# Optimization experiments

Measured on AMD Instinct MI355X. Metric: run time of the kernel, lower is better.

Reference implementation:

```python
import jax, jax.numpy as jnp
import numpy as np

MAXDISP = 25               # module stores maxdisp + 1
OFFSET = (MAXDISP - 1) // 2  # center of the residual disparity range


def setup_inputs() -> dict:
    key = jax.random.key(0)
    k1, k2 = jax.random.split(key)
    x = jax.random.normal(k1, (8, 32, 256, 512), dtype=jnp.float32)
    y = jax.random.normal(k2, (8, 32, 256, 512), dtype=jnp.float32)
    return {"x": x, "y": y}


def reference(x, y):
    # Residual cost volume: for each centered disparity shift d, the cost slice
    # is the channel-wise L1 distance between x and y shifted by d along width,
    # with zeros in the out-of-overlap columns.
    N, C, H, W = x.shape
    slices = []
    for i in range(MAXDISP):  # small fixed loop over disparity hypotheses
        d = i - OFFSET
        if d < 0:
            # overlap occupies columns [0, W+d); right -d columns are zero
            c = jnp.abs(x[..., : W + d] - y[..., -d:]).sum(axis=1)
            c = jnp.pad(c, ((0, 0), (0, 0), (0, -d)))
        elif d > 0:
            # overlap occupies columns [d, W); left d columns are zero
            c = jnp.abs(x[..., d:] - y[..., : W - d]).sum(axis=1)
            c = jnp.pad(c, ((0, 0), (0, 0), (d, 0)))
        else:
            c = jnp.abs(x - y).sum(axis=1)
        slices.append(c)  # (N, H, W)
    return jnp.stack(slices, axis=1)  # (N, MAXDISP, H, W)
```

## Files before the change

kernel.cpp:

```cpp
#include <hip/hip_runtime.h>

namespace {
constexpr int N_ = 8, C_ = 32, H_ = 256, W_ = 512, DISP_ = 25;
constexpr int CH = H_ * W_;
constexpr int TILE = 256;
constexpr int NSS = C_ / 2;
constexpr int YST = 288;
constexpr int YOFF = 256;
constexpr int BUF = 560;
}

typedef __attribute__((ext_vector_type(2))) _Float16 h2;

__device__ __forceinline__ h2 u2h(unsigned u) { return __builtin_bit_cast(h2, u); }
__device__ __forceinline__ unsigned h2u(h2 v) { return __builtin_bit_cast(unsigned, v); }

template <int G>
__device__ __forceinline__ void body(const float* px, const float* py0,
                                     const float* py1, bool extra,
                                     float* __restrict__ op, unsigned* lds,
                                     int tid, int w0l, int w0g) {
  constexpr int I0 = (G == 0) ? 0 : (G == 1) ? 7 : (G == 2) ? 13 : 19;
  constexpr int NI = (G == 0) ? 7 : 6;
  constexpr int OFF = (G == 0) ? 4 : (G == 1) ? 0 : (G == 2) ? -8 : -12;

  const h2 one = {(_Float16)1.0f, (_Float16)1.0f};

  float acc[NI][4];
#pragma unroll
  for (int il = 0; il < NI; ++il)
#pragma unroll
    for (int cw = 0; cw < 4; ++cw) acc[il][cw] = 0.0f;

  float a0, a1, b0, b1, c0, c1;

#define SLOAD()                                                           \
  do {                                                                    \
    a0 = px[0]; a1 = px[CH];                                              \
    b0 = py0[0]; b1 = py0[CH];                                            \
    if (extra) { c0 = py1[0]; c1 = py1[CH]; }                             \
    px += 2 * CH; py0 += 2 * CH; py1 += 2 * CH;                           \
  } while (0)

#define SWRITE(bsel)                                                      \
  do {                                                                    \
    unsigned* wp = lds + (bsel)*BUF;                                      \
    h2 pa = __builtin_bit_cast(h2, __builtin_amdgcn_cvt_pkrtz(a0, a1));   \
    h2 pb = __builtin_bit_cast(h2, __builtin_amdgcn_cvt_pkrtz(b0, b1));   \
    wp[tid] = h2u(pa);                                                    \
    wp[YOFF + tid] = h2u(pb);                                             \
    if (extra) {                                                          \
      h2 pc = __builtin_bit_cast(h2, __builtin_amdgcn_cvt_pkrtz(c0, c1)); \
      wp[YOFF + 256 + tid] = h2u(pc);                                     \
    }                                                                     \
  } while (0)

#define COMPUTE(bsel)                                                     \
  do {                                                                    \
    const unsigned* bp = lds + (bsel)*BUF;                                \
    const uint4 xq = *reinterpret_cast<const uint4*>(bp + w0l);           \
    const uint4 q0 = *reinterpret_cast<const uint4*>(bp + YOFF + w0l +    \
                                                     (OFF + 12));         \
    const uint4 q1 = *reinterpret_cast<const uint4*>(bp + YOFF + w0l +    \
                                                     (OFF + 12) + 4);    \
    const uint4 q2 = *reinterpret_cast<const uint4*>(bp + YOFF + w0l +    \
                                                     (OFF + 12) + 8);    \
    const unsigned xs[4] = {xq.x, xq.y, xq.z, xq.w};                      \
    const unsigned yw[12] = {q0.x, q0.y, q0.z, q0.w, q1.x, q1.y, q1.z,    \
                             q1.w, q2.x, q2.y, q2.z, q2.w};               \
    _Pragma("unroll") for (int il = 0; il < NI; ++il) {                   \
      _Pragma("unroll") for (int cw = 0; cw < 4; ++cw) {                  \
        h2 d = u2h(xs[cw]) - u2h(yw[cw + 12 - (I0 + il) - OFF]);          \
        h2 a = u2h(h2u(d) & 0x7FFF7FFFu);                                 \
        acc[il][cw] = __builtin_amdgcn_fdot2(a, one, acc[il][cw], false); \
      }                                                                   \
    }                                                                     \
  } while (0)

  SLOAD();
  SWRITE(0);
  __syncthreads();

  int cb = 0;
#pragma unroll 1
  for (int s = 0; s < NSS; ++s) {
    const bool more = (s + 1 < NSS);
    if (more) SLOAD();
    COMPUTE(cb);
    if (more) SWRITE(cb ^ 1);
    __syncthreads();
    cb ^= 1;
  }

#undef SLOAD
#undef SWRITE
#undef COMPUTE

#pragma unroll
  for (int il = 0; il < NI; ++il) {
    const int i = I0 + il;
    const int j0 = w0g - i + 12;
    float4 v;
    v.x = ((unsigned)(j0 + 0) < (unsigned)W_) ? acc[il][0] : 0.0f;
    v.y = ((unsigned)(j0 + 1) < (unsigned)W_) ? acc[il][1] : 0.0f;
    v.z = ((unsigned)(j0 + 2) < (unsigned)W_) ? acc[il][2] : 0.0f;
    v.w = ((unsigned)(j0 + 3) < (unsigned)W_) ? acc[il][3] : 0.0f;
    *reinterpret_cast<float4*>(op + (size_t)i * CH) = v;
  }
}

__global__ __launch_bounds__(256, 5) void rescost_kernel(
    const float* __restrict__ x, const float* __restrict__ y,
    float* __restrict__ out) {
  __shared__ __align__(16) unsigned lds[2 * BUF];

  const int tid = threadIdx.x;
  const int tl = tid & 63;
  const int g = tid >> 6;
  const int bid = blockIdx.x;
  const int tile = bid & 1;
  const int r = bid >> 1;
  const int n = r >> 8;
  const int h = r & (H_ - 1);
  const int tb = tile * TILE;
  const int w0l = tl << 2;
  const int w0g = tb + w0l;

  const size_t row_base = ((size_t)n * C_ * H_ + (size_t)h) * W_;

  const int gx = tb + tid;
  int gy0 = tb - 12 + tid;
  gy0 = gy0 < 0 ? 0 : (gy0 > W_ - 1 ? W_ - 1 : gy0);
  int gy1 = tb - 12 + 256 + tid;
  gy1 = gy1 < 0 ? 0 : (gy1 > W_ - 1 ? W_ - 1 : gy1);
  const bool extra = tid < (YST - 256);

  const float* px = x + row_base + gx;
  const float* py0 = y + row_base + gy0;
  const float* py1 = y + row_base + gy1;
  float* op = out + (size_t)n * DISP_ * CH + (size_t)h * W_ + w0g;

  if (g == 0)
    body<0>(px, py0, py1, extra, op, lds, tid, w0l, w0g);
  else if (g == 1)
    body<1>(px, py0, py1, extra, op, lds, tid, w0l, w0g);
  else if (g == 2)
    body<2>(px, py0, py1, extra, op, lds, tid, w0l, w0g);
  else
    body<3>(px, py0, py1, extra, op, lds, tid, w0l, w0g);
}

extern "C" void kernel_launch(void* const* d_in, const int* in_sizes, int n_in,
                              void* d_out, int out_size, void* d_ws, size_t ws_size,
                              hipStream_t stream) {
  const float* x = (const float*)d_in[0];
  const float* y = (const float*)d_in[1];
  float* out = (float*)d_out;
  dim3 grid(N_ * H_ * 2);
  dim3 block(256);
  hipLaunchKernelGGL(rescost_kernel, grid, block, 0, stream, x, y, out);
}
```

Baseline: 81.31 us.

## Load x directly from global as float4 and stage only y in LDS

```diff
diff --git a/kernel.cpp b/kernel.cpp
--- a/kernel.cpp
+++ b/kernel.cpp
@@ -4,26 +4,30 @@
 constexpr int N_ = 8, C_ = 32, H_ = 256, W_ = 512, DISP_ = 25;
 constexpr int CH = H_ * W_;
 constexpr int TILE = 256;
-constexpr int NSS = C_ / 2;
+constexpr int NSS = C_ / 4;
 constexpr int YST = 288;
-constexpr int YOFF = 256;
-constexpr int BUF = 560;
+constexpr int BUFU = 2 * YST;
 }
 
 typedef __attribute__((ext_vector_type(2))) _Float16 h2;
 
-__device__ __forceinline__ h2 u2h(unsigned u) { return __builtin_bit_cast(h2, u); }
-__device__ __forceinline__ unsigned h2u(h2 v) { return __builtin_bit_cast(unsigned, v); }
+static __device__ __forceinline__ h2 u2h(unsigned u) {
+  return __builtin_bit_cast(h2, u);
+}
+static __device__ __forceinline__ unsigned pk(float a, float b) {
+  return __builtin_bit_cast(unsigned, __builtin_amdgcn_cvt_pkrtz(a, b));
+}
 
 template <int G>
-__device__ __forceinline__ void body(const float* px, const float* py0,
-                                     const float* py1, bool extra,
+__device__ __forceinline__ void body(const float* xb, const float* yj0,
+                                     const float* yj1, const float* yj2,
+                                     bool e2, int wj0, int wj1, int wj2,
                                      float* __restrict__ op, unsigned* lds,
-                                     int tid, int w0l, int w0g) {
+                                     int w0l, int w0g) {
   constexpr int I0 = (G == 0) ? 0 : (G == 1) ? 7 : (G == 2) ? 13 : 19;
   constexpr int NI = (G == 0) ? 7 : 6;
   constexpr int OFF = (G == 0) ? 4 : (G == 1) ? 0 : (G == 2) ? -8 : -12;
-
+  const int jb = w0l + (OFF + 12);
   const h2 one = {(_Float16)1.0f, (_Float16)1.0f};
 
   float acc[NI][4];
@@ -32,68 +36,84 @@
 #pragma unroll
     for (int cw = 0; cw < 4; ++cw) acc[il][cw] = 0.0f;
 
-  float a0, a1, b0, b1, c0, c1;
+  float4 xl0, xl1, xl2, xl3;
+  float ya0, ya1, yb0, yb1, yc0, yc1;
 
-#define SLOAD()                                                           \
+#define YLOAD(s)                                                          \
   do {                                                                    \
-    a0 = px[0]; a1 = px[CH];                                              \
-    b0 = py0[0]; b1 = py0[CH];                                            \
-    if (extra) { c0 = py1[0]; c1 = py1[CH]; }                             \
-    px += 2 * CH; py0 += 2 * CH; py1 += 2 * CH;                           \
-  } while (0)
-
-#define SWRITE(bsel)                                                      \
-  do {                                                                    \
-    unsigned* wp = lds + (bsel)*BUF;                                      \
-    h2 pa = __builtin_bit_cast(h2, __builtin_amdgcn_cvt_pkrtz(a0, a1));   \
-    h2 pb = __builtin_bit_cast(h2, __builtin_amdgcn_cvt_pkrtz(b0, b1));   \
-    wp[tid] = h2u(pa);                                                    \
-    wp[YOFF + tid] = h2u(pb);                                             \
-    if (extra) {                                                          \
-      h2 pc = __builtin_bit_cast(h2, __builtin_amdgcn_cvt_pkrtz(c0, c1)); \
-      wp[YOFF + 256 + tid] = h2u(pc);                                     \
+    const float* b0 = yj0 + (size_t)(s) * 4 * CH;                         \
+    ya0 = b0[0]; ya1 = b0[CH];                                            \
+    const float* b1 = yj1 + (size_t)(s) * 4 * CH;                         \
+    yb0 = b1[0]; yb1 = b1[CH];                                            \
+    if (e2) {                                                             \
+      const float* b2 = yj2 + (size_t)(s) * 4 * CH;                       \
+      yc0 = b2[0]; yc1 = b2[CH];                                          \
     }                                                                     \
   } while (0)
 
-#define COMPUTE(bsel)                                                     \
+#define YWRITE(buf)                                                       \
   do {                                                                    \
-    const unsigned* bp = lds + (bsel)*BUF;                                \
-    const uint4 xq = *reinterpret_cast<const uint4*>(bp + w0l);           \
-    const uint4 q0 = *reinterpret_cast<const uint4*>(bp + YOFF + w0l +    \
-                                                     (OFF + 12));         \
-    const uint4 q1 = *reinterpret_cast<const uint4*>(bp + YOFF + w0l +    \
-                                                     (OFF + 12) + 4);    \
-    const uint4 q2 = *reinterpret_cast<const uint4*>(bp + YOFF + w0l +    \
-                                                     (OFF + 12) + 8);    \
-    const unsigned xs[4] = {xq.x, xq.y, xq.z, xq.w};                      \
-    const unsigned yw[12] = {q0.x, q0.y, q0.z, q0.w, q1.x, q1.y, q1.z,    \
-                             q1.w, q2.x, q2.y, q2.z, q2.w};               \
-    _Pragma("unroll") for (int il = 0; il < NI; ++il) {                   \
-      _Pragma("unroll") for (int cw = 0; cw < 4; ++cw) {                  \
-        h2 d = u2h(xs[cw]) - u2h(yw[cw + 12 - (I0 + il) - OFF]);          \
-        h2 a = u2h(h2u(d) & 0x7FFF7FFFu);                                 \
-        acc[il][cw] = __builtin_amdgcn_fdot2(a, one, acc[il][cw], false); \
+    unsigned* wp = lds + (buf)*BUFU;                                      \
+    wp[wj0] = pk(ya0, ya1);                                               \
+    wp[wj1] = pk(yb0, yb1);                                               \
+    if (e2) wp[wj2] = pk(yc0, yc1);                                       \
+  } while (0)
+
+#define XLOAD(s)                                                          \
+  do {                                                                    \
+    const float* xc = xb + (size_t)(s) * 4 * CH;                          \
+    xl0 = *reinterpret_cast<const float4*>(xc);                           \
+    xl1 = *reinterpret_cast<const float4*>(xc + CH);                      \
+    xl2 = *reinterpret_cast<const float4*>(xc + 2 * CH);                  \
+    xl3 = *reinterpret_cast<const float4*>(xc + 3 * CH);                  \
+  } while (0)
+
+#define COMPUTE(buf)                                                      \
+  do {                                                                    \
+    const unsigned xpk0[4] = {pk(xl0.x, xl1.x), pk(xl0.y, xl1.y),         \
+                              pk(xl0.z, xl1.z), pk(xl0.w, xl1.w)};        \
+    const unsigned xpk1[4] = {pk(xl2.x, xl3.x), pk(xl2.y, xl3.y),         \
+                              pk(xl2.z, xl3.z), pk(xl2.w, xl3.w)};        \
+    const unsigned* bp = lds + (buf)*BUFU;                                \
+    _Pragma("unroll") for (int p = 0; p < 2; ++p) {                       \
+      const unsigned* yp = bp + p * YST + jb;                             \
+      const uint4 q0 = *reinterpret_cast<const uint4*>(yp);               \
+      const uint4 q1 = *reinterpret_cast<const uint4*>(yp + 4);           \
+      const uint4 q2 = *reinterpret_cast<const uint4*>(yp + 8);           \
+      const unsigned yw[12] = {q0.x, q0.y, q0.z, q0.w, q1.x, q1.y,        \
+                               q1.z, q1.w, q2.x, q2.y, q2.z, q2.w};       \
+      const unsigned* xq = p ? xpk1 : xpk0;                               \
+      _Pragma("unroll") for (int il = 0; il < NI; ++il) {                 \
+        _Pragma("unroll") for (int cw = 0; cw < 4; ++cw) {                \
+          h2 d = u2h(xq[cw]) - u2h(yw[cw + 12 - OFF - (I0 + il)]);        \
+          h2 a = u2h(__builtin_bit_cast(unsigned, d) & 0x7FFF7FFFu);      \
+          acc[il][cw] = __builtin_amdgcn_fdot2(a, one, acc[il][cw], false);\
+        }                                                                 \
       }                                                                   \
     }                                                                     \
   } while (0)
 
-  SLOAD();
-  SWRITE(0);
-  __syncthreads();
+  YLOAD(0);
+  XLOAD(0);
+  YWRITE(0);
+  asm volatile("s_waitcnt lgkmcnt(0)" ::: "memory");
+  __builtin_amdgcn_s_barrier();
 
-  int cb = 0;
 #pragma unroll 1
   for (int s = 0; s < NSS; ++s) {
-    const bool more = (s + 1 < NSS);
-    if (more) SLOAD();
-    COMPUTE(cb);
-    if (more) SWRITE(cb ^ 1);
-    __syncthreads();
-    cb ^= 1;
+    if (s + 1 < NSS) YLOAD(s + 1);
+    COMPUTE(s & 1);
+    if (s + 1 < NSS) {
+      XLOAD(s + 1);
+      YWRITE((s + 1) & 1);
+    }
+    asm volatile("s_waitcnt lgkmcnt(0)" ::: "memory");
+    __builtin_amdgcn_s_barrier();
   }
 
-#undef SLOAD
-#undef SWRITE
+#undef YLOAD
+#undef YWRITE
+#undef XLOAD
 #undef COMPUTE
 
 #pragma unroll
@@ -109,10 +129,10 @@
   }
 }
 
-__global__ __launch_bounds__(256, 5) void rescost_kernel(
+__global__ __launch_bounds__(256, 4) void rescost_kernel(
     const float* __restrict__ x, const float* __restrict__ y,
     float* __restrict__ out) {
-  __shared__ __align__(16) unsigned lds[2 * BUF];
+  __shared__ __align__(16) unsigned lds[2 * BUFU];
 
   const int tid = threadIdx.x;
   const int tl = tid & 63;
@@ -128,26 +148,33 @@
 
   const size_t row_base = ((size_t)n * C_ * H_ + (size_t)h) * W_;
 
-  const int gx = tb + tid;
-  int gy0 = tb - 12 + tid;
-  gy0 = gy0 < 0 ? 0 : (gy0 > W_ - 1 ? W_ - 1 : gy0);
-  int gy1 = tb - 12 + 256 + tid;
-  gy1 = gy1 < 0 ? 0 : (gy1 > W_ - 1 ? W_ - 1 : gy1);
-  const bool extra = tid < (YST - 256);
+  const int p1 = (tid >= 32) ? 1 : 0;
+  const int jc0 = tid;
+  const int jc1 = tid + 256 - p1 * YST;
+  const int jc2 = tid + 512 - YST;
+  const bool e2 = (tid < 64);
 
-  const float* px = x + row_base + gx;
-  const float* py0 = y + row_base + gy0;
-  const float* py1 = y + row_base + gy1;
+  auto yclamp = [&](int jc) {
+    int c = tb - 12 + jc;
+    c = c < 0 ? 0 : (c > W_ - 1 ? W_ - 1 : c);
+    return c;
+  };
+  const float* yj0 = y + row_base + yclamp(jc0);
+  const float* yj1 = y + row_base + yclamp(jc1) + p1 * 2 * CH;
+  const float* yj2 = y + row_base + yclamp(jc2) + 2 * CH;
+  const int wj0 = tid, wj1 = tid + 256, wj2 = tid + 512;
+
+  const float* xb = x + row_base + w0g;
   float* op = out + (size_t)n * DISP_ * CH + (size_t)h * W_ + w0g;
 
   if (g == 0)
-    body<0>(px, py0, py1, extra, op, lds, tid, w0l, w0g);
+    body<0>(xb, yj0, yj1, yj2, e2, wj0, wj1, wj2, op, lds, w0l, w0g);
   else if (g == 1)
-    body<1>(px, py0, py1, extra, op, lds, tid, w0l, w0g);
+    body<1>(xb, yj0, yj1, yj2, e2, wj0, wj1, wj2, op, lds, w0l, w0g);
   else if (g == 2)
-    body<2>(px, py0, py1, extra, op, lds, tid, w0l, w0g);
+    body<2>(xb, yj0, yj1, yj2, e2, wj0, wj1, wj2, op, lds, w0l, w0g);
   else
-    body<3>(px, py0, py1, extra, op, lds, tid, w0l, w0g);
+    body<3>(xb, yj0, yj1, yj2, e2, wj0, wj1, wj2, op, lds, w0l, w0g);
 }
 
 extern "C" void kernel_launch(void* const* d_in, const int* in_sizes, int n_in,
```

Result: slower. 84.31 us (+3.7%).
